# Kernel tuning notes

Hardware: AMD Instinct MI355X
Metric: run time of the kernel (lower is better)

The kernel has to match this reference:

```python
import jax, jax.numpy as jnp
import numpy as np

N, S, M = 16, 256, 768
TK, HA = 10, 1          # tK stages, hA heads (from RTM.__init__)
DH = M // HA
EPS = 1e-5
WSCALE = 0.02           # scale on randn weights to keep 10 stacked stages numerically sane


def _pos_bias():
    # bias[i][j][z] = sin(j / 10000**(2z/M)), bias[i][j][z+1] = cos(...); independent of i
    pos = np.arange(S, dtype=np.float64)[:, None]
    z = np.arange(0, M, 2, dtype=np.float64)
    ang = pos / (10000.0 ** (2.0 * z / M))          # (S, M/2)
    pe = np.zeros((S, M), dtype=np.float32)
    pe[:, 0::2] = np.sin(ang)
    pe[:, 1::2] = np.cos(ang)
    return jnp.asarray(pe)

PE = _pos_bias()


def _ln(v, g, b):
    mu = jnp.mean(v, axis=-1, keepdims=True)
    var = jnp.var(v, axis=-1, keepdims=True)
    return (v - mu) / jnp.sqrt(var + EPS) * g + b


def setup_inputs() -> dict:
    key = jax.random.key(0)
    ks = jax.random.split(key, 8)
    rn = lambda k, shp: jax.random.normal(k, shp, dtype=jnp.float32)
    return {
        "x": rn(ks[0], (N, S, M)),
        "weight": rn(ks[1], (M, M)) * WSCALE,
        "Wq": rn(ks[2], (TK, HA, DH, M)) * WSCALE,
        "Wk": rn(ks[3], (TK, HA, DH, M)) * WSCALE,
        "Wv": rn(ks[4], (TK, HA, DH, M)) * WSCALE,
        "Wo": rn(ks[5], (TK, M, M)) * WSCALE,
        "ln1_g": jnp.ones((M,), jnp.float32), "ln1_b": jnp.zeros((M,), jnp.float32),
        "ln2_g": jnp.ones((M,), jnp.float32), "ln2_b": jnp.zeros((M,), jnp.float32),
        "fc1_w": rn(ks[6], (4 * M, M)) * WSCALE, "fc1_b": jnp.zeros((4 * M,), jnp.float32),
        "fc2_w": rn(ks[7], (M, 4 * M)) * WSCALE, "fc2_b": jnp.zeros((M,), jnp.float32),
    }


def reference(x, weight, Wq, Wk, Wv, Wo, ln1_g, ln1_b, ln2_g, ln2_b,
              fc1_w, fc1_b, fc2_w, fc2_b):
    # savespace[i,j] = weight @ x[i,j,:]  (x[j,:,i] after the double transpose), + sin/cos bias
    s0 = jnp.einsum('mn,ijn->ijm', weight, x) + PE[None, :, :]   # (N, S, M)
    inv_sqrt_dh = jnp.float32(1.0 / np.sqrt(DH))

    def mlp(s):
        h = jax.nn.gelu(s @ fc1_w.T + fc1_b, approximate=False)
        return h @ fc2_w.T + fc2_b

    # Sequential over tokens j: token j attends (strictly causal) to the per-stage V
    # of all previous tokens, accumulated in cumV. Within a token, the tK stages run
    # sequentially, each mutating the token's state s (as the torch code mutates savespace).
    def token_step(cumV, s):                # cumV: (TK, N, HA, DH); s: (N, M)
        newV = []
        for a in range(TK):
            sn = _ln(s, ln1_g, ln1_b)
            q = jnp.einsum('hdm,nm->nhd', Wq[a], sn)
            k = jnp.einsum('hdm,nm->nhd', Wk[a], sn)
            v = jnp.einsum('hdm,nm->nhd', Wv[a], sn)
            logit = jnp.sum(q * inv_sqrt_dh * k, axis=-1)                # (N, HA) scalar score
            rsa = jax.nn.softmax(logit[..., None], axis=-1)[..., 0]      # softmax of scalar == 1
            imv = cumV[a]                                                # (N, HA, DH): sum_{subj<j}
            s = jnp.einsum('mk,nk->nm', Wo[a], imv.reshape(N, HA * DH)) + s
            s = _ln(s, ln2_g, ln2_b) + s
            s = mlp(s)
            newV.append(rsa[..., None] * v)
        return cumV + jnp.stack(newV, axis=0), s

    cumV0 = jnp.zeros((TK, N, HA, DH), x.dtype)
    _, ys = jax.lax.scan(token_step, cumV0, jnp.swapaxes(s0, 0, 1))      # ys: (S, N, M)
    return jnp.swapaxes(ys, 0, 1)                                        # (N, S, M)
```

## Files before the change

kernel.cpp:

```cpp
#include <hip/hip_runtime.h>
#include <hip/hip_bf16.h>
#include <math.h>


using bf16   = __bf16;
using bf16x8 = __attribute__((ext_vector_type(8))) __bf16;
using f32x4  = __attribute__((ext_vector_type(4))) float;

#define DEV __device__ __forceinline__

DEV void gload16(const bf16* g, bf16* l) {
  __builtin_amdgcn_global_load_lds(
      (const __attribute__((address_space(1))) unsigned int*)g,
      (__attribute__((address_space(3))) unsigned int*)l, 16, 0, 0);
}

DEV float gelu_f(float x) {
  const float y  = x * 0.70710678118654752f;
  const float ay = fabsf(y);
  const float t  = __builtin_amdgcn_rcpf(__builtin_fmaf(0.3275911f, ay, 1.0f));
  float p = __builtin_fmaf(1.061405429f, t, -1.453152027f);
  p = __builtin_fmaf(p, t, 1.421413741f);
  p = __builtin_fmaf(p, t, -0.284496736f);
  p = __builtin_fmaf(p, t, 0.254829592f);
  p = p * t;
  const float e = __expf(-ay * ay);
  float er = __builtin_fmaf(-p, e, 1.0f);
  er = __builtin_copysignf(er, y);
  return 0.5f * x * (1.0f + er);
}

enum { EPI_PART = 0, EPI_GELU = 1, EPI_B16 = 2 };

template <int BN, int EPI>
__global__ __launch_bounds__(256) void gemm_k(
    const bf16* __restrict__ A, const bf16* __restrict__ B,
    float* __restrict__ outF, bf16* __restrict__ outB,
    const float* __restrict__ aux, int K, int N,
    int kZ, int klen, size_t aZ, size_t bZ, size_t oZ)
{
  constexpr int ABUF = 128 * 32;
  constexpr int BBUF = BN * 32;
  __shared__ bf16 As[3 * ABUF];
  __shared__ bf16 Bs[3 * BBUF];
  const int z = blockIdx.z;
  A += (size_t)z * aZ;
  B += (size_t)z * bZ;
  const int kbeg = z * kZ;
  const int tid  = threadIdx.x;
  const int lane = tid & 63, wave = tid >> 6;
  const int m0 = blockIdx.x * 128, n0 = blockIdx.y * BN;

  const int r  = tid >> 2;
  const int kq = ((tid & 3) - (tid >> 3)) & 3;
  const bf16* aG0 = A + (size_t)(m0 + r) * K + kq * 8 + kbeg;
  const bf16* aG1 = aG0 + (size_t)64 * K;
  const bf16* bG0 = B + (size_t)(n0 + r) * K + kq * 8 + kbeg;
  const bf16* bG1 = bG0 + (size_t)64 * K;

  const int wr = (wave & 1) * 64, wc = (wave >> 1) * (BN / 2);
  const int lr = lane & 15, kb = lane >> 4;
  const int swz  = ((kb + (lr >> 1)) & 3) * 8;
  const int aOff = (wr + lr) * 32 + swz;
  const int bOff = (wc + lr) * 32 + swz;

  constexpr int MT = 4, NT = BN / 32;
  f32x4 acc[MT][NT] = {};
  const int iters = klen >> 5;

  auto stage = [&](int p, int k0) {
    bf16* aD = &As[p * ABUF + tid * 8];
    gload16(aG0 + k0, aD);
    gload16(aG1 + k0, aD + 2048);
    bf16* bD = &Bs[p * BBUF + tid * 8];
    gload16(bG0 + k0, bD);
    if (BN == 128) gload16(bG1 + k0, bD + 2048);
  };

  stage(0, 0);
  if (iters > 1) stage(1, 32);
  int cur = 0, nxt = 2;
  for (int it = 0; it < iters; ++it) {
    if (it + 1 < iters) {
      if constexpr (BN == 128) asm volatile("s_waitcnt vmcnt(4)" ::: "memory");
      else                     asm volatile("s_waitcnt vmcnt(3)" ::: "memory");
    } else {
      asm volatile("s_waitcnt vmcnt(0)" ::: "memory");
    }
    __builtin_amdgcn_s_barrier();
    asm volatile("" ::: "memory");
    if (it + 2 < iters) stage(nxt, (it + 2) * 32);
    asm volatile("" ::: "memory");
    const int pa = cur * ABUF, pb = cur * BBUF;
    bf16x8 af[MT], bfv[NT];
#pragma unroll
    for (int t = 0; t < MT; ++t) af[t] = *(const bf16x8*)&As[pa + aOff + t * 512];
#pragma unroll
    for (int t = 0; t < NT; ++t) bfv[t] = *(const bf16x8*)&Bs[pb + bOff + t * 512];
#pragma unroll
    for (int mt = 0; mt < MT; ++mt)
#pragma unroll
      for (int nt = 0; nt < NT; ++nt)
        acc[mt][nt] = __builtin_amdgcn_mfma_f32_16x16x32_bf16(af[mt], bfv[nt], acc[mt][nt], 0, 0, 0);
    cur = (cur == 2) ? 0 : cur + 1;
    nxt = (nxt == 2) ? 0 : nxt + 1;
  }

  const int row0 = m0 + wr + (lane >> 4) * 4;
  const int col0 = n0 + wc + lr;
  float* oF = (EPI == EPI_PART) ? outF + (size_t)z * oZ : nullptr;
  bf16*  oB = (EPI == EPI_B16)  ? outB + (size_t)z * oZ : outB;
#pragma unroll
  for (int mt = 0; mt < MT; ++mt) {
#pragma unroll
    for (int nt = 0; nt < NT; ++nt) {
      const int col = col0 + nt * 16;
      float bias = 0.f;
      if (EPI == EPI_GELU) bias = aux[col];
#pragma unroll
      for (int rg = 0; rg < 4; ++rg) {
        const int row = row0 + mt * 16 + rg;
        float v = acc[mt][nt][rg];
        if (EPI == EPI_PART) {
          oF[(size_t)row * N + col] = v;
        } else if (EPI == EPI_GELU) {
          oB[(size_t)row * N + col] = (bf16)gelu_f(v + bias);
        } else {
          oB[(size_t)row * N + col] = (bf16)v;
        }
      }
    }
  }
}

template <int NP, int MODE>
__global__ __launch_bounds__(256) void reduce_ln(
    const float* __restrict__ P, size_t pZ,
    const float* __restrict__ add, const float* __restrict__ g,
    const float* __restrict__ b, float* __restrict__ Tout,
    bf16* __restrict__ SNout)
{
  const int row = blockIdx.x, t = threadIdx.x;
  float v[3];
#pragma unroll
  for (int c = 0; c < 3; ++c) {
    const int col = t + c * 256;
    float s = P[(size_t)row * 768 + col];
#pragma unroll
    for (int p = 1; p < NP; ++p) s += P[(size_t)p * pZ + (size_t)row * 768 + col];
    if (MODE == 0) s += add[(row & 255) * 768 + col];
    if (MODE == 1) s += add[(size_t)row * 768 + col];
    if (MODE == 2 || MODE == 3) s += add[col];
    v[c] = s;
  }
  if (MODE != 1) {
#pragma unroll
    for (int c = 0; c < 3; ++c) Tout[(size_t)row * 768 + t + c * 256] = v[c];
  }
  if (MODE == 3) return;

  __shared__ float red[8];
  float s = v[0] + v[1] + v[2];
#pragma unroll
  for (int o = 32; o >= 1; o >>= 1) s += __shfl_down(s, o);
  if ((t & 63) == 0) red[t >> 6] = s;
  __syncthreads();
  const float mu = (red[0] + red[1] + red[2] + red[3]) * (1.f / 768.f);
  const float d0 = v[0] - mu, d1 = v[1] - mu, d2 = v[2] - mu;
  float q = d0 * d0 + d1 * d1 + d2 * d2;
#pragma unroll
  for (int o = 32; o >= 1; o >>= 1) q += __shfl_down(q, o);
  if ((t & 63) == 0) red[4 + (t >> 6)] = q;
  __syncthreads();
  const float var = (red[4] + red[5] + red[6] + red[7]) * (1.f / 768.f);
  const float rs = rsqrtf(var + 1e-5f);
  float y0 = d0 * rs * g[t] + b[t];
  float y1 = d1 * rs * g[t + 256] + b[t + 256];
  float y2 = d2 * rs * g[t + 512] + b[t + 512];
  if (MODE == 1) { y0 += v[0]; y1 += v[1]; y2 += v[2]; }
  bf16* o = SNout + (size_t)row * 768;
  o[t] = (bf16)y0; o[t + 256] = (bf16)y1; o[t + 512] = (bf16)y2;
}

__global__ __launch_bounds__(256) void scan_partial_b(
    const bf16* __restrict__ SN, float* __restrict__ Ps)
{
  const int n = blockIdx.x, ch = blockIdx.y, d = blockIdx.z * 256 + threadIdx.x;
  const bf16* base = SN + ((size_t)(n * 256 + ch * 16)) * 768 + d;
  float s = 0.f;
#pragma unroll
  for (int j = 0; j < 16; ++j) s += (float)base[(size_t)j * 768];
  Ps[(size_t)(n * 16 + ch) * 768 + d] = s;
}

__global__ __launch_bounds__(256) void scan_final_b(
    const bf16* __restrict__ SN, const float* __restrict__ Ps,
    bf16* __restrict__ PSb)
{
  const int n = blockIdx.x, ch = blockIdx.y, d = blockIdx.z * 256 + threadIdx.x;
  float run = 0.f;
  for (int c = 0; c < ch; ++c) run += Ps[(size_t)(n * 16 + c) * 768 + d];
  const bf16* vb = SN + ((size_t)(n * 256 + ch * 16)) * 768 + d;
  bf16* ob = PSb + ((size_t)(n * 256 + ch * 16)) * 768 + d;
#pragma unroll
  for (int j = 0; j < 16; ++j) {
    ob[(size_t)j * 768] = (bf16)run;
    run += (float)vb[(size_t)j * 768];
  }
}

__global__ __launch_bounds__(256) void transpose_wv(
    const float* __restrict__ Wv, bf16* __restrict__ WvT)
{
  __shared__ float tile[64][65];
  const int a = blockIdx.z, k0 = blockIdx.x * 64, n0 = blockIdx.y * 64;
  const int c = threadIdx.x & 63, r4 = threadIdx.x >> 6;
  const float* src = Wv + (size_t)a * 589824;
  bf16* dst = WvT + (size_t)a * 589824;
#pragma unroll
  for (int i = 0; i < 16; ++i)
    tile[r4 + i * 4][c] = src[(size_t)(k0 + r4 + i * 4) * 768 + n0 + c];
  __syncthreads();
#pragma unroll
  for (int i = 0; i < 16; ++i) {
    const int n = r4 + i * 4;
    dst[(size_t)(n0 + n) * 768 + k0 + c] = (bf16)tile[c][n];
  }
}

__global__ __launch_bounds__(256) void f32_to_bf16_k(
    const float* __restrict__ in, bf16* __restrict__ out, int n4)
{
  const int i = blockIdx.x * 256 + threadIdx.x;
  if (i >= n4) return;
  const float4 v = ((const float4*)in)[i];
  bf16 h[4] = {(bf16)v.x, (bf16)v.y, (bf16)v.z, (bf16)v.w};
  *(uint2*)(out + 4 * (size_t)i) = *(uint2*)h;
}

__global__ __launch_bounds__(256) void pe_kernel(float* __restrict__ PE)
{
  const int id = blockIdx.x * 256 + threadIdx.x;
  const int j = id / 384, p = id % 384;
  const double ang = (double)j * pow(10000.0, -4.0 * (double)p / 768.0);
  PE[(size_t)j * 768 + 2 * p]     = (float)sin(ang);
  PE[(size_t)j * 768 + 2 * p + 1] = (float)cos(ang);
}

extern "C" void kernel_launch(void* const* d_in, const int* in_sizes, int n_in,
                              void* d_out, int out_size, void* d_ws, size_t ws_size,
                              hipStream_t stream)
{
  const float* x      = (const float*)d_in[0];
  const float* weight = (const float*)d_in[1];
  const float* Wv     = (const float*)d_in[4];
  const float* Wo     = (const float*)d_in[5];
  const float* ln1g   = (const float*)d_in[6];
  const float* ln1b   = (const float*)d_in[7];
  const float* ln2g   = (const float*)d_in[8];
  const float* ln2b   = (const float*)d_in[9];
  const float* fc1w   = (const float*)d_in[10];
  const float* fc1b   = (const float*)d_in[11];
  const float* fc2w   = (const float*)d_in[12];
  const float* fc2b   = (const float*)d_in[13];
  float* out = (float*)d_out;

  char* p = (char*)d_ws;
  auto alloc = [&](size_t bytes) { char* r = p; p += (bytes + 255) & ~(size_t)255; return r; };
  bf16*  Wb_w  = (bf16*)alloc(589824ull * 2);
  bf16*  Wb_o  = (bf16*)alloc(5898240ull * 2);
  bf16*  WvT   = (bf16*)alloc(5898240ull * 2);
  bf16*  Wvo   = (bf16*)alloc(5898240ull * 2);
  bf16*  Wb_f1 = (bf16*)alloc(2359296ull * 2);
  bf16*  Wb_f2 = (bf16*)alloc(2359296ull * 2);
  bf16*  Xb    = (bf16*)alloc(3145728ull * 2);
  float* PEf   = (float*)alloc(196608ull * 4);
  float* T     = (float*)alloc(3145728ull * 4);
  bf16*  SN    = (bf16*)alloc(3145728ull * 2);
  bf16*  PSb   = (bf16*)alloc(3145728ull * 2);
  bf16*  H     = (bf16*)alloc(12582912ull * 2);
  float* Ps    = (float*)alloc(196608ull * 4);
  float* Part  = (float*)alloc(2ull * 3145728ull * 4);

  auto cvt = [&](const float* src, bf16* dst, int n) {
    int n4 = n / 4;
    f32_to_bf16_k<<<(n4 + 255) / 256, 256, 0, stream>>>(src, dst, n4);
  };
  cvt(x, Xb, 3145728);
  cvt(weight, Wb_w, 589824);
  cvt(Wo, Wb_o, 5898240);
  cvt(fc1w, Wb_f1, 2359296);
  cvt(fc2w, Wb_f2, 2359296);
  transpose_wv<<<dim3(12, 12, 10), 256, 0, stream>>>(Wv, WvT);
  pe_kernel<<<384, 256, 0, stream>>>(PEf);

  gemm_k<128, EPI_B16><<<dim3(6, 6, 10), 256, 0, stream>>>(
      Wb_o, WvT, nullptr, Wvo, nullptr, 768, 768, 0, 768, 589824, 589824, 589824);

  gemm_k<64, EPI_PART><<<dim3(32, 12, 2), 256, 0, stream>>>(
      Xb, Wb_w, Part, nullptr, nullptr, 768, 768, 384, 384, 0, 0, 3145728);
  reduce_ln<2, 0><<<4096, 256, 0, stream>>>(Part, 3145728, PEf, ln1g, ln1b, T, SN);

  for (int a = 0; a < 10; ++a) {
    scan_partial_b<<<dim3(16, 16, 3), 256, 0, stream>>>(SN, Ps);
    scan_final_b<<<dim3(16, 16, 3), 256, 0, stream>>>(SN, Ps, PSb);
    gemm_k<64, EPI_PART><<<dim3(32, 12, 2), 256, 0, stream>>>(
        PSb, Wvo + (size_t)a * 589824, Part, nullptr, nullptr, 768, 768, 384, 384, 0, 0, 3145728);
    reduce_ln<2, 1><<<4096, 256, 0, stream>>>(Part, 3145728, T, ln2g, ln2b, nullptr, SN);
    gemm_k<128, EPI_GELU><<<dim3(32, 24, 1), 256, 0, stream>>>(
        SN, Wb_f1, nullptr, H, fc1b, 768, 3072, 0, 768, 0, 0, 0);
    gemm_k<64, EPI_PART><<<dim3(32, 12, 2), 256, 0, stream>>>(
        H, Wb_f2, Part, nullptr, nullptr, 3072, 768, 1536, 1536, 0, 0, 3145728);
    if (a < 9)
      reduce_ln<2, 2><<<4096, 256, 0, stream>>>(Part, 3145728, fc2b, ln1g, ln1b, T, SN);
    else
      reduce_ln<2, 3><<<4096, 256, 0, stream>>>(Part, 3145728, fc2b, nullptr, nullptr, out, nullptr);
  }
  (void)in_sizes; (void)n_in; (void)out_size; (void)ws_size;
}
```

Before: 1.263 ms.

## Add 256x256-tile 512-thread GEMM for MLP fc1/fc2 with 4-way split-K

Adds a new GEMM kernel that uses 256x256 tiles, 8 waves, a 4-stage LDS ring with interleaved A/B staging, workgroup swizzling and raised MFMA priority. The fc1 (GELU epilogue) and fc2 GEMMs in each stage move onto it, and fc2 goes from 2-way to 4-way split-K, so the partial buffer and reduce_ln now sum 4 partials. The goal is more data reuse per tile and better latency hiding for the two largest per-stage GEMMs. In exchange the fc1 grid shrinks to 192 blocks, which may underfill the GPU, and the reduction reads twice as many partials.

```diff
diff --git a/kernel.cpp b/kernel.cpp
--- a/kernel.cpp
+++ b/kernel.cpp
@@ -31,6 +31,128 @@
 }
 
 enum { EPI_PART = 0, EPI_GELU = 1, EPI_B16 = 2 };
+
+template <int EPI>
+__global__ __launch_bounds__(512, 2) void gemm256(
+    const bf16* __restrict__ A, const bf16* __restrict__ B,
+    float* __restrict__ outF, bf16* __restrict__ outB,
+    const float* __restrict__ aux, int K, int N,
+    int kZ, int klen, size_t oZ)
+{
+  constexpr int TBUF = 256 * 32;
+  __shared__ bf16 As[4 * TBUF];
+  __shared__ bf16 Bs[4 * TBUF];
+  const int z = blockIdx.z;
+  const int kbeg = z * kZ;
+  const int tid = threadIdx.x, lane = tid & 63, w = tid >> 6;
+  const int wr = w >> 2, wc = w & 3;
+
+  const int nx = gridDim.x;
+  const int nwg = nx * (int)gridDim.y;
+  int f = blockIdx.x + nx * blockIdx.y;
+  f = (f & 7) * (nwg >> 3) + (f >> 3);
+  const int m0 = (f % nx) * 256, n0 = (f / nx) * 256;
+
+  const int r  = tid >> 2;
+  const int kq = ((tid & 3) - (tid >> 3)) & 3;
+  const bf16* aG0 = A + (size_t)(m0 + r) * K + kq * 8 + kbeg;
+  const bf16* aG1 = aG0 + (size_t)128 * K;
+  const bf16* bG0 = B + (size_t)(n0 + r) * K + kq * 8 + kbeg;
+  const bf16* bG1 = bG0 + (size_t)128 * K;
+
+  const int lr = lane & 15, kb = lane >> 4;
+  const int swz   = ((kb + (lr >> 1)) & 3) * 8;
+  const int aBase = (wr * 128 + lr) * 32 + swz;
+  const int bBase = (wc * 64 + lr) * 32 + swz;
+
+  f32x4 acc[8][4] = {};
+  const int NT = klen >> 5;
+
+  auto stageA = [&](int buf, int t) {
+    bf16* d = &As[buf * TBUF + tid * 8];
+    gload16(aG0 + t * 32, d);
+    gload16(aG1 + t * 32, d + 4096);
+  };
+  auto stageB = [&](int buf, int t) {
+    bf16* d = &Bs[buf * TBUF + tid * 8];
+    gload16(bG0 + t * 32, d);
+    gload16(bG1 + t * 32, d + 4096);
+  };
+
+  stageA(0, 0); stageB(0, 0);
+  if (NT > 1) { stageA(1, 1); stageB(1, 1); }
+  if (NT > 2) { stageA(2, 2); stageB(2, 2); }
+  if (NT > 2)      asm volatile("s_waitcnt vmcnt(8)" ::: "memory");
+  else if (NT > 1) asm volatile("s_waitcnt vmcnt(4)" ::: "memory");
+  else             asm volatile("s_waitcnt vmcnt(0)" ::: "memory");
+  __builtin_amdgcn_s_barrier();
+  asm volatile("" ::: "memory");
+
+  for (int t = 0; t < NT; ++t) {
+    const int pa = (t & 3) * TBUF;
+    bf16x8 af[4], bfv[4];
+#pragma unroll
+    for (int g = 0; g < 4; ++g) af[g] = *(const bf16x8*)&As[pa + aBase + g * 512];
+#pragma unroll
+    for (int nt = 0; nt < 4; ++nt) bfv[nt] = *(const bf16x8*)&Bs[pa + bBase + nt * 512];
+    if (t + 3 < NT) stageA((t + 3) & 3, t + 3);
+    asm volatile("" ::: "memory");
+    __builtin_amdgcn_s_barrier();
+    asm volatile("" ::: "memory");
+    __builtin_amdgcn_s_setprio(1);
+#pragma unroll
+    for (int g = 0; g < 4; ++g)
+#pragma unroll
+      for (int nt = 0; nt < 4; ++nt)
+        acc[g][nt] = __builtin_amdgcn_mfma_f32_16x16x32_bf16(af[g], bfv[nt], acc[g][nt], 0, 0, 0);
+    __builtin_amdgcn_s_setprio(0);
+    asm volatile("" ::: "memory");
+    __builtin_amdgcn_s_barrier();
+    asm volatile("" ::: "memory");
+#pragma unroll
+    for (int g = 0; g < 4; ++g) af[g] = *(const bf16x8*)&As[pa + aBase + 2048 + g * 512];
+    if (t + 3 < NT) stageB((t + 3) & 3, t + 3);
+    asm volatile("" ::: "memory");
+    __builtin_amdgcn_s_barrier();
+    asm volatile("" ::: "memory");
+    __builtin_amdgcn_s_setprio(1);
+#pragma unroll
+    for (int g = 0; g < 4; ++g)
+#pragma unroll
+      for (int nt = 0; nt < 4; ++nt)
+        acc[4 + g][nt] = __builtin_amdgcn_mfma_f32_16x16x32_bf16(af[g], bfv[nt], acc[4 + g][nt], 0, 0, 0);
+    __builtin_amdgcn_s_setprio(0);
+    if (t + 3 < NT)      asm volatile("s_waitcnt vmcnt(8)" ::: "memory");
+    else if (t + 2 < NT) asm volatile("s_waitcnt vmcnt(4)" ::: "memory");
+    else if (t + 1 < NT) asm volatile("s_waitcnt vmcnt(0)" ::: "memory");
+    asm volatile("" ::: "memory");
+    __builtin_amdgcn_s_barrier();
+    asm volatile("" ::: "memory");
+  }
+
+  const int row0 = m0 + wr * 128 + (lane >> 4) * 4;
+  const int col0 = n0 + wc * 64 + lr;
+  float* oF = (EPI == EPI_PART) ? outF + (size_t)z * oZ : nullptr;
+#pragma unroll
+  for (int mt = 0; mt < 8; ++mt) {
+#pragma unroll
+    for (int nt = 0; nt < 4; ++nt) {
+      const int col = col0 + nt * 16;
+      float bias = 0.f;
+      if (EPI == EPI_GELU) bias = aux[col];
+#pragma unroll
+      for (int rg = 0; rg < 4; ++rg) {
+        const int row = row0 + mt * 16 + rg;
+        float v = acc[mt][nt][rg];
+        if (EPI == EPI_PART) {
+          oF[(size_t)row * N + col] = v;
+        } else {
+          outB[(size_t)row * N + col] = (bf16)gelu_f(v + bias);
+        }
+      }
+    }
+  }
+}
 
 template <int BN, int EPI>
 __global__ __launch_bounds__(256) void gemm_k(
@@ -280,7 +402,7 @@
   bf16*  PSb   = (bf16*)alloc(3145728ull * 2);
   bf16*  H     = (bf16*)alloc(12582912ull * 2);
   float* Ps    = (float*)alloc(196608ull * 4);
-  float* Part  = (float*)alloc(2ull * 3145728ull * 4);
+  float* Part  = (float*)alloc(4ull * 3145728ull * 4);
 
   auto cvt = [&](const float* src, bf16* dst, int n) {
     int n4 = n / 4;
@@ -307,14 +429,14 @@
     gemm_k<64, EPI_PART><<<dim3(32, 12, 2), 256, 0, stream>>>(
         PSb, Wvo + (size_t)a * 589824, Part, nullptr, nullptr, 768, 768, 384, 384, 0, 0, 3145728);
     reduce_ln<2, 1><<<4096, 256, 0, stream>>>(Part, 3145728, T, ln2g, ln2b, nullptr, SN);
-    gemm_k<128, EPI_GELU><<<dim3(32, 24, 1), 256, 0, stream>>>(
-        SN, Wb_f1, nullptr, H, fc1b, 768, 3072, 0, 768, 0, 0, 0);
-    gemm_k<64, EPI_PART><<<dim3(32, 12, 2), 256, 0, stream>>>(
-        H, Wb_f2, Part, nullptr, nullptr, 3072, 768, 1536, 1536, 0, 0, 3145728);
+    gemm256<EPI_GELU><<<dim3(16, 12, 1), 512, 0, stream>>>(
+        SN, Wb_f1, nullptr, H, fc1b, 768, 3072, 0, 768, 0);
+    gemm256<EPI_PART><<<dim3(16, 3, 4), 512, 0, stream>>>(
+        H, Wb_f2, Part, nullptr, nullptr, 3072, 768, 768, 768, 3145728);
     if (a < 9)
-      reduce_ln<2, 2><<<4096, 256, 0, stream>>>(Part, 3145728, fc2b, ln1g, ln1b, T, SN);
+      reduce_ln<4, 2><<<4096, 256, 0, stream>>>(Part, 3145728, fc2b, ln1g, ln1b, T, SN);
     else
-      reduce_ln<2, 3><<<4096, 256, 0, stream>>>(Part, 3145728, fc2b, nullptr, nullptr, out, nullptr);
+      reduce_ln<4, 3><<<4096, 256, 0, stream>>>(Part, 3145728, fc2b, nullptr, nullptr, out, nullptr);
   }
   (void)in_sizes; (void)n_in; (void)out_size; (void)ws_size;
 }
```

After: 1.369 ms. 8.4% more time.
